# Performance work log

Hardware: AMD Instinct MI355X
Metric: run time of the kernel (lower is better)

The kernel has to match this reference:

```python
import jax, jax.numpy as jnp
import numpy as np

BATCH, SEQ, DIM = 4, 4096, 1024


def setup_inputs() -> dict:
    key = jax.random.key(0)
    ks = jax.random.split(key, 7)
    return {
        "x": jax.random.normal(ks[0], (BATCH, SEQ, DIM), dtype=jnp.float32),
        "phazor_re": jax.random.normal(ks[1], (DIM,), dtype=jnp.float32),
        "phazor_im": jax.random.normal(ks[2], (DIM,), dtype=jnp.float32),
        "phazor_init_re": jax.random.normal(ks[3], (DIM,), dtype=jnp.float32),
        "phazor_init_im": jax.random.normal(ks[4], (DIM,), dtype=jnp.float32),
        "last_conv_re": jax.random.normal(ks[5], (BATCH, DIM), dtype=jnp.float32),
        "last_conv_im": jax.random.normal(ks[6], (BATCH, DIM), dtype=jnp.float32),
    }


def reference(x, phazor_re, phazor_im, phazor_init_re, phazor_init_im,
              last_conv_re, last_conv_im):
    L = x.shape[1]
    phazor_p = phazor_re + 1j * phazor_im                      # raw param (dim,)
    phazor_init = phazor_init_re + 1j * phazor_init_im          # (dim,)
    last_conv = last_conv_re + 1j * last_conv_im                # (batch, dim)

    mag = jnp.abs(phazor_p)
    phazor = phazor_p / mag * jnp.exp(-mag)                     # (dim,) |phazor|<1
    t = jnp.arange(L)[:, None]                                  # (L,1)
    phazor_prog = jnp.power(phazor[None, :], t)                 # (L, dim) = phazor^t
    filt = phazor_prog * phazor_init[None, :]                   # (L, dim)

    filt_fft = jnp.fft.fft(filt, n=2 * L, axis=0)               # (2L, dim)
    x_fft = jnp.fft.fft(x.astype(jnp.complex64), n=2 * L, axis=1)  # (B, 2L, dim)
    conv = jnp.fft.ifft(filt_fft[None] * x_fft, axis=1)[:, :L]  # (B, L, dim)

    # add decayed initial state: last_conv * phazor^(t+1)
    conv = conv + last_conv[:, None, :] * phazor_prog[None] * phazor[None, None, :]
    return conv.real
```

## Files before the change

### kernel.cpp

```cpp
#include <hip/hip_runtime.h>


#define BB 4
#define LL 4096
#define DD 1024
#define CHUNK 16
#define KK 256
#define SEG 32
#define NSEG 8
#define NBLK 1024u

__device__ __forceinline__ void phazor_of(float pr, float pi, float& ar, float& ai) {
    float mag = sqrtf(pr * pr + pi * pi);
    float s = expf(-mag) / mag;
    ar = pr * s;
    ai = pi * s;
}

__device__ __forceinline__ void csq(float& r, float& i) {
    float nr = r * r - i * i;
    i = 2.f * r * i;
    r = nr;
}

__device__ __forceinline__ void st8(float2* p, float2 v) {
    __hip_atomic_store(p, v, __ATOMIC_RELAXED, __HIP_MEMORY_SCOPE_AGENT);
}
__device__ __forceinline__ float2 ld8(const float2* p) {
    return __hip_atomic_load((float2*)p, __ATOMIC_RELAXED, __HIP_MEMORY_SCOPE_AGENT);
}

__device__ __forceinline__ void grid_barrier(unsigned* A, unsigned* G) {
    __syncthreads();
    if (threadIdx.x == 0) {
        const unsigned g = blockIdx.x >> 5;
        unsigned a = __hip_atomic_fetch_add(&A[g * 32], 1u,
                        __ATOMIC_RELAXED, __HIP_MEMORY_SCOPE_AGENT);
        if (a == 31u)
            __hip_atomic_fetch_add(G, 32u,
                        __ATOMIC_RELAXED, __HIP_MEMORY_SCOPE_AGENT);
        long long spins = 0;
        while (__hip_atomic_load(G, __ATOMIC_RELAXED,
                                 __HIP_MEMORY_SCOPE_AGENT) < NBLK) {
            __builtin_amdgcn_s_sleep(32);
            if (++spins > (1LL << 22)) break;
        }
    }
    __syncthreads();
}

__global__ __launch_bounds__(256, 4) void spiral_fused(
    const float* __restrict__ x,
    const float* __restrict__ p_re, const float* __restrict__ p_im,
    const float* __restrict__ in_re, const float* __restrict__ in_im,
    const float* __restrict__ lc_re, const float* __restrict__ lc_im,
    float2* __restrict__ S, float2* __restrict__ R, float2* __restrict__ T,
    unsigned* __restrict__ bar,
    float* __restrict__ out)
{
    const int tid = blockIdx.x * 256 + threadIdx.x;
    const int dq = tid & (DD / 4 - 1);
    const int k  = (tid >> 8) & (KK - 1);
    const int b  = tid >> 16;
    const int d0 = dq * 4;

    float ar[4], ai[4], br[4], bi[4];
    {
        float4 prv = *(const float4*)(p_re + d0);
        float4 piv = *(const float4*)(p_im + d0);
        float4 brv = *(const float4*)(in_re + d0);
        float4 biv = *(const float4*)(in_im + d0);
        float prs[4] = {prv.x, prv.y, prv.z, prv.w};
        float pis[4] = {piv.x, piv.y, piv.z, piv.w};
        br[0] = brv.x; br[1] = brv.y; br[2] = brv.z; br[3] = brv.w;
        bi[0] = biv.x; bi[1] = biv.y; bi[2] = biv.z; bi[3] = biv.w;
#pragma unroll
        for (int q = 0; q < 4; ++q) phazor_of(prs[q], pis[q], ar[q], ai[q]);
    }

    const size_t xbase = (size_t)(b * LL + k * CHUNK) * DD + d0;

    {
        const float* xp = x + xbase;
        float4 xv[16];
#pragma unroll
        for (int j = 0; j < 16; ++j)
            xv[j] = *(const float4*)(xp + (size_t)j * DD);

        float sr[4] = {0.f, 0.f, 0.f, 0.f};
        float si[4] = {0.f, 0.f, 0.f, 0.f};
#pragma unroll
        for (int j = 0; j < 16; ++j) {
            float xs[4] = {xv[j].x, xv[j].y, xv[j].z, xv[j].w};
#pragma unroll
            for (int q = 0; q < 4; ++q) {
                float nr = fmaf(ar[q], sr[q], fmaf(-ai[q], si[q], br[q] * xs[q]));
                float ni = fmaf(ar[q], si[q], fmaf( ai[q], sr[q], bi[q] * xs[q]));
                sr[q] = nr; si[q] = ni;
            }
        }
        float2* Sp = S + ((size_t)(b * KK + k) * DD + d0);
#pragma unroll
        for (int q = 0; q < 4; ++q)
            st8(Sp + q, make_float2(sr[q], si[q]));
    }

    grid_barrier(bar, bar + 1024);

    if (blockIdx.x < 128) {
        const int gt  = tid;
        const int d   = gt & (DD - 1);
        const int seg = (gt >> 10) & (NSEG - 1);
        const int bb  = gt >> 13;

        float qr, qi;
        phazor_of(p_re[d], p_im[d], qr, qi);
#pragma unroll
        for (int i = 0; i < 4; ++i) csq(qr, qi);

        const int kk0 = seg * SEG;
        const float2* Sc = S + ((size_t)bb * KK * DD + d);
        float2*       Rc = R + ((size_t)bb * KK * DD + d);

        float2 buf[8];
#pragma unroll
        for (int j = 0; j < 8; ++j) buf[j] = ld8(Sc + (size_t)(kk0 + j) * DD);

        float cr = 0.f, ci = 0.f;
        for (int i = 0; i < SEG; i += 8) {
#pragma unroll
            for (int j = 0; j < 8; ++j) {
                st8(Rc + (size_t)(kk0 + i + j) * DD, make_float2(cr, ci));
                float2 s = buf[j];
                int kn = i + j + 8;
                buf[j] = ld8(Sc + (size_t)(kk0 + (kn < SEG ? kn : SEG - 1)) * DD);
                float nr = fmaf(qr, cr, fmaf(-qi, ci, s.x));
                float ni = fmaf(qr, ci, fmaf( qi, cr, s.y));
                cr = nr; ci = ni;
            }
        }
        st8(T + ((size_t)bb * NSEG + seg) * DD + d, make_float2(cr, ci));
    }

    grid_barrier(bar + 2048, bar + 3072);

    const int rel  = k & (SEG - 1);
    const int seg3 = k >> 5;

    float gr[4], gi[4];
    {
        float4 lrv = *(const float4*)(lc_re + b * DD + d0);
        float4 liv = *(const float4*)(lc_im + b * DD + d0);
        gr[0] = lrv.x; gr[1] = lrv.y; gr[2] = lrv.z; gr[3] = lrv.w;
        gi[0] = liv.x; gi[1] = liv.y; gi[2] = liv.z; gi[3] = liv.w;
        float Qr[4], Qi[4];
#pragma unroll
        for (int q = 0; q < 4; ++q) {
            Qr[q] = ar[q]; Qi[q] = ai[q];
#pragma unroll
            for (int i = 0; i < 9; ++i) csq(Qr[q], Qi[q]);
        }
        for (int s = 0; s < seg3; ++s) {
            const float2* Tp = T + ((size_t)(b * NSEG + s) * DD + d0);
#pragma unroll
            for (int q = 0; q < 4; ++q) {
                float2 t = ld8(Tp + q);
                float nr = fmaf(Qr[q], gr[q], fmaf(-Qi[q], gi[q], t.x));
                float ni = fmaf(Qr[q], gi[q], fmaf( Qi[q], gr[q], t.y));
                gr[q] = nr; gi[q] = ni;
            }
        }
    }

    float cr[4], ci[4];
    {
        const float2* Rp = R + ((size_t)(b * KK + k) * DD + d0);
#pragma unroll
        for (int q = 0; q < 4; ++q) {
            float qdr = ar[q], qdi = ai[q];
#pragma unroll
            for (int i = 0; i < 4; ++i) csq(qdr, qdi);
            float pr = 1.f, pi = 0.f;
            float bpr = qdr, bpi = qdi;
#pragma unroll
            for (int bit = 0; bit < 5; ++bit) {
                if ((rel >> bit) & 1) {
                    float nr = pr * bpr - pi * bpi;
                    pi = pr * bpi + pi * bpr;
                    pr = nr;
                }
                csq(bpr, bpi);
            }
            float2 r = ld8(Rp + q);
            cr[q] = r.x + pr * gr[q] - pi * gi[q];
            ci[q] = r.y + pr * gi[q] + pi * gr[q];
        }
    }

    {
        const float* xp = x + xbase;
        float* op = out + xbase;
        float4 xv[16];
#pragma unroll
        for (int j = 0; j < 16; ++j)
            xv[j] = *(const float4*)(xp + (size_t)j * DD);
#pragma unroll
        for (int j = 0; j < 16; ++j) {
            float xs[4] = {xv[j].x, xv[j].y, xv[j].z, xv[j].w};
            float os[4];
#pragma unroll
            for (int q = 0; q < 4; ++q) {
                float nr = fmaf(ar[q], cr[q], fmaf(-ai[q], ci[q], br[q] * xs[q]));
                float ni = fmaf(ar[q], ci[q], fmaf( ai[q], cr[q], bi[q] * xs[q]));
                cr[q] = nr; ci[q] = ni;
                os[q] = nr;
            }
            *(float4*)(op + (size_t)j * DD) = make_float4(os[0], os[1], os[2], os[3]);
        }
    }
}

extern "C" void kernel_launch(void* const* d_in, const int* in_sizes, int n_in,
                              void* d_out, int out_size, void* d_ws, size_t ws_size,
                              hipStream_t stream) {
    const float* x      = (const float*)d_in[0];
    const float* p_re   = (const float*)d_in[1];
    const float* p_im   = (const float*)d_in[2];
    const float* pin_re = (const float*)d_in[3];
    const float* pin_im = (const float*)d_in[4];
    const float* lc_re  = (const float*)d_in[5];
    const float* lc_im  = (const float*)d_in[6];
    float* out = (float*)d_out;

    char* ws = (char*)d_ws;
    float2*   S   = (float2*)(ws);
    float2*   R   = (float2*)(ws + (size_t)8  * 1024 * 1024);
    float2*   T   = (float2*)(ws + (size_t)16 * 1024 * 1024);
    unsigned* bar = (unsigned*)(ws + (size_t)17 * 1024 * 1024);

    hipMemsetAsync(bar, 0, 16384, stream);

    spiral_fused<<<dim3(NBLK), dim3(256), 0, stream>>>(
        x, p_re, p_im, pin_re, pin_im, lc_re, lc_im, S, R, T, bar, out);
}
```

Baseline: 159.7 us.

## Cache half of x tile in LDS, prefetch rest, use generation-counted barriers

The barrier counters move to persistent __device__ globals with generation counting, so the per-launch hipMemsetAsync on the workspace is dropped. Half of each thread's 16-row x tile is kept in shared memory across the grid barriers. The other half is reloaded right after the second barrier so the load overlaps the carry computation, which removes most of the second global read of x. In exchange, 32 KB of LDS per block may lower occupancy, and the barrier spin timeout is shortened.

```diff
diff --git a/kernel.cpp b/kernel.cpp
--- a/kernel.cpp
+++ b/kernel.cpp
@@ -10,6 +10,9 @@
 #define NSEG 8
 #define NBLK 1024u
 
+__device__ unsigned g_grp[2 * 32 * 32];
+__device__ unsigned g_glob[2 * 32];
+
 __device__ __forceinline__ void phazor_of(float pr, float pi, float& ar, float& ai) {
     float mag = sqrtf(pr * pr + pi * pi);
     float s = expf(-mag) / mag;
@@ -30,20 +33,23 @@
     return __hip_atomic_load((float2*)p, __ATOMIC_RELAXED, __HIP_MEMORY_SCOPE_AGENT);
 }
 
-__device__ __forceinline__ void grid_barrier(unsigned* A, unsigned* G) {
+__device__ __forceinline__ void grid_barrier(int site) {
     __syncthreads();
     if (threadIdx.x == 0) {
-        const unsigned g = blockIdx.x >> 5;
-        unsigned a = __hip_atomic_fetch_add(&A[g * 32], 1u,
+        unsigned* A = &g_grp[site * 1024 + (blockIdx.x >> 5) * 32];
+        unsigned* G = &g_glob[site * 32];
+        unsigned a = __hip_atomic_fetch_add(A, 1u,
                         __ATOMIC_RELAXED, __HIP_MEMORY_SCOPE_AGENT);
-        if (a == 31u)
+        unsigned gen = a >> 5;
+        if ((a & 31u) == 31u)
             __hip_atomic_fetch_add(G, 32u,
                         __ATOMIC_RELAXED, __HIP_MEMORY_SCOPE_AGENT);
-        long long spins = 0;
-        while (__hip_atomic_load(G, __ATOMIC_RELAXED,
-                                 __HIP_MEMORY_SCOPE_AGENT) < NBLK) {
-            __builtin_amdgcn_s_sleep(32);
-            if (++spins > (1LL << 22)) break;
+        unsigned target = (gen + 1u) * NBLK;
+        int spins = 0;
+        while ((int)(__hip_atomic_load(G, __ATOMIC_RELAXED,
+                                       __HIP_MEMORY_SCOPE_AGENT) - target) < 0) {
+            __builtin_amdgcn_s_sleep(16);
+            if (++spins > (1 << 17)) break;
         }
     }
     __syncthreads();
@@ -55,9 +61,10 @@
     const float* __restrict__ in_re, const float* __restrict__ in_im,
     const float* __restrict__ lc_re, const float* __restrict__ lc_im,
     float2* __restrict__ S, float2* __restrict__ R, float2* __restrict__ T,
-    unsigned* __restrict__ bar,
     float* __restrict__ out)
 {
+    __shared__ float4 xlds[8][256];
+
     const int tid = blockIdx.x * 256 + threadIdx.x;
     const int dq = tid & (DD / 4 - 1);
     const int k  = (tid >> 8) & (KK - 1);
@@ -87,6 +94,10 @@
         for (int j = 0; j < 16; ++j)
             xv[j] = *(const float4*)(xp + (size_t)j * DD);
 
+#pragma unroll
+        for (int j = 0; j < 8; ++j)
+            xlds[j][threadIdx.x] = xv[j];
+
         float sr[4] = {0.f, 0.f, 0.f, 0.f};
         float si[4] = {0.f, 0.f, 0.f, 0.f};
 #pragma unroll
@@ -105,7 +116,7 @@
             st8(Sp + q, make_float2(sr[q], si[q]));
     }
 
-    grid_barrier(bar, bar + 1024);
+    grid_barrier(0);
 
     if (blockIdx.x < 128) {
         const int gt  = tid;
@@ -142,10 +153,18 @@
         st8(T + ((size_t)bb * NSEG + seg) * DD + d, make_float2(cr, ci));
     }
 
-    grid_barrier(bar + 2048, bar + 3072);
+    grid_barrier(1);
 
     const int rel  = k & (SEG - 1);
     const int seg3 = k >> 5;
+
+    float4 xv2[8];
+    {
+        const float* xp = x + xbase;
+#pragma unroll
+        for (int j = 0; j < 8; ++j)
+            xv2[j] = *(const float4*)(xp + (size_t)(8 + j) * DD);
+    }
 
     float gr[4], gi[4];
     {
@@ -198,15 +217,11 @@
     }
 
     {
-        const float* xp = x + xbase;
         float* op = out + xbase;
-        float4 xv[16];
-#pragma unroll
-        for (int j = 0; j < 16; ++j)
-            xv[j] = *(const float4*)(xp + (size_t)j * DD);
-#pragma unroll
-        for (int j = 0; j < 16; ++j) {
-            float xs[4] = {xv[j].x, xv[j].y, xv[j].z, xv[j].w};
+#pragma unroll
+        for (int j = 0; j < 8; ++j) {
+            float4 xj = xlds[j][threadIdx.x];
+            float xs[4] = {xj.x, xj.y, xj.z, xj.w};
             float os[4];
 #pragma unroll
             for (int q = 0; q < 4; ++q) {
@@ -216,6 +231,19 @@
                 os[q] = nr;
             }
             *(float4*)(op + (size_t)j * DD) = make_float4(os[0], os[1], os[2], os[3]);
+        }
+#pragma unroll
+        for (int j = 0; j < 8; ++j) {
+            float xs[4] = {xv2[j].x, xv2[j].y, xv2[j].z, xv2[j].w};
+            float os[4];
+#pragma unroll
+            for (int q = 0; q < 4; ++q) {
+                float nr = fmaf(ar[q], cr[q], fmaf(-ai[q], ci[q], br[q] * xs[q]));
+                float ni = fmaf(ar[q], ci[q], fmaf( ai[q], cr[q], bi[q] * xs[q]));
+                cr[q] = nr; ci[q] = ni;
+                os[q] = nr;
+            }
+            *(float4*)(op + (size_t)(8 + j) * DD) = make_float4(os[0], os[1], os[2], os[3]);
         }
     }
 }
@@ -233,13 +261,10 @@
     float* out = (float*)d_out;
 
     char* ws = (char*)d_ws;
-    float2*   S   = (float2*)(ws);
-    float2*   R   = (float2*)(ws + (size_t)8  * 1024 * 1024);
-    float2*   T   = (float2*)(ws + (size_t)16 * 1024 * 1024);
-    unsigned* bar = (unsigned*)(ws + (size_t)17 * 1024 * 1024);
-
-    hipMemsetAsync(bar, 0, 16384, stream);
+    float2* S = (float2*)(ws);
+    float2* R = (float2*)(ws + (size_t)8  * 1024 * 1024);
+    float2* T = (float2*)(ws + (size_t)16 * 1024 * 1024);
 
     spiral_fused<<<dim3(NBLK), dim3(256), 0, stream>>>(
-        x, p_re, p_im, pin_re, pin_im, lc_re, lc_im, S, R, T, bar, out);
-}
+        x, p_re, p_im, pin_re, pin_im, lc_re, lc_im, S, R, T, out);
+}
```

Measured after the change: 155.4 us. 1.03x faster.
